# Kernel optimization log

Measured on AMD Instinct MI355X. Metric: run time of the kernel, lower is better.

## Reference

```python
import jax, jax.numpy as jnp
import numpy as np

N = 100000   # nodes
E = 1600000  # edges
G = 512      # graphs in batch
F_IN = 128
H = 128
F_OUT = 1


def setup_inputs() -> dict:
    key = jax.random.key(0)
    ks = jax.random.split(key, 12)
    x = jax.random.normal(ks[0], (N, F_IN), dtype=jnp.float32)
    src = jax.random.randint(ks[1], (E,), 0, N, dtype=jnp.int32)
    dst = jax.random.randint(ks[2], (E,), 0, N, dtype=jnp.int32)
    node2graph = jnp.sort(jax.random.randint(ks[3], (N,), 0, G, dtype=jnp.int32))
    s_in = 1.0 / np.sqrt(F_IN)
    s_h = 1.0 / np.sqrt(H)
    W0 = jax.random.normal(ks[4], (F_IN, H), dtype=jnp.float32) * s_in
    b0 = jnp.zeros((H,), dtype=jnp.float32)
    W1 = jax.random.normal(ks[5], (H, H), dtype=jnp.float32) * s_h
    b1 = jnp.zeros((H,), dtype=jnp.float32)
    W2 = jax.random.normal(ks[6], (H, H), dtype=jnp.float32) * s_h
    b2 = jnp.zeros((H,), dtype=jnp.float32)
    Wm1 = jax.random.normal(ks[7], (H, H), dtype=jnp.float32) * s_h
    bm1 = jnp.zeros((H,), dtype=jnp.float32)
    Wm2 = jax.random.normal(ks[8], (H, F_OUT), dtype=jnp.float32) * s_h
    bm2 = jnp.zeros((F_OUT,), dtype=jnp.float32)
    return {"x": x, "src": src, "dst": dst, "node2graph": node2graph,
            "W0": W0, "b0": b0, "W1": W1, "b1": b1, "W2": W2, "b2": b2,
            "Wm1": Wm1, "bm1": bm1, "Wm2": Wm2, "bm2": bm2}


def _degree_norms(src, dst):
    ones = jnp.ones((E,), dtype=jnp.float32)
    out_deg = jax.ops.segment_sum(ones, src, num_segments=N)
    in_deg = jax.ops.segment_sum(ones, dst, num_segments=N)
    norm_out = jax.lax.rsqrt(jnp.maximum(out_deg, 1.0))  # [N]
    norm_in = jax.lax.rsqrt(jnp.maximum(in_deg, 1.0))    # [N]
    return norm_out, norm_in


def _graph_conv(x, src, dst, norm_out, norm_in, W, b):
    # DGL GraphConv, norm='both', in_feats <= out_feats path:
    # aggregate normalized src features, then linear + activation.
    xs = x * norm_out[:, None]
    msg = xs[src]                                         # [E, H] gather
    agg = jax.ops.segment_sum(msg, dst, num_segments=N)   # [N, H] scatter-add
    agg = agg * norm_in[:, None]
    return jax.nn.relu(agg @ W + b)


def reference(x, src, dst, node2graph, W0, b0, W1, b1, W2, b2, Wm1, bm1, Wm2, bm2):
    norm_out, norm_in = _degree_norms(src, dst)
    h = _graph_conv(x, src, dst, norm_out, norm_in, W0, b0)
    h = _graph_conv(h, src, dst, norm_out, norm_in, W1, b1)
    h = _graph_conv(h, src, dst, norm_out, norm_in, W2, b2)
    # sum_nodes readout per graph
    g = jax.ops.segment_sum(h, node2graph, num_segments=G)  # [G, H]
    # MLP head: Linear -> ReLU -> Linear
    return jax.nn.relu(g @ Wm1 + bm1) @ Wm2 + bm2           # [G, 1]
```

## Files before the change

### kernel.cpp

```cpp
#include <hip/hip_runtime.h>

#define NN 100000
#define NE 1600000
#define NG 512
#define HD 128

#define NBK 196
#define CHUNK 5120
#define NC 313
#define LH (2 * NBK * NC)

typedef _Float16 half4 __attribute__((ext_vector_type(4)));
typedef _Float16 h8 __attribute__((ext_vector_type(8)));
typedef float f32x4 __attribute__((ext_vector_type(4)));

__global__ __launch_bounds__(256) void k_hist(const int* __restrict__ src,
                                              const int* __restrict__ dst,
                                              int* __restrict__ H,
                                              const float* __restrict__ W0,
                                              const float* __restrict__ W1,
                                              const float* __restrict__ W2,
                                              _Float16* __restrict__ Bt) {
    if (blockIdx.x >= NC) {
        int i = (blockIdx.x - NC) * 256 + threadIdx.x;
        int w = i >> 14;
        int rem = i & 16383;
        int n = rem >> 7;
        int k = rem & 127;
        const float* W = (w == 0) ? W0 : ((w == 1) ? W1 : W2);
        Bt[i] = (_Float16)W[k * 128 + n];
        return;
    }
    __shared__ int hd[NBK], hs[NBK];
    int c = blockIdx.x;
    for (int i = threadIdx.x; i < NBK; i += 256) { hd[i] = 0; hs[i] = 0; }
    __syncthreads();
    int e0 = c * CHUNK;
    int e1 = e0 + CHUNK; if (e1 > NE) e1 = NE;
    for (int e = e0 + threadIdx.x; e < e1; e += 256) {
        atomicAdd(&hd[dst[e] >> 9], 1);
        atomicAdd(&hs[src[e] >> 9], 1);
    }
    __syncthreads();
    for (int i = threadIdx.x; i < NBK; i += 256) {
        H[i * NC + c] = hd[i];
        H[NBK * NC + i * NC + c] = hs[i];
    }
}

__global__ __launch_bounds__(256) void k_scan1g(int* __restrict__ H,
                                                int* __restrict__ bsum, int L) {
    __shared__ int s[256];
    int i = blockIdx.x * 256 + threadIdx.x;
    int v = (i < L) ? H[i] : 0;
    s[threadIdx.x] = v;
    __syncthreads();
    for (int off = 1; off < 256; off <<= 1) {
        int t = (threadIdx.x >= off) ? s[threadIdx.x - off] : 0;
        __syncthreads();
        s[threadIdx.x] += t;
        __syncthreads();
    }
    if (i < L) H[i] = s[threadIdx.x] - v;
    if (threadIdx.x == 255) bsum[blockIdx.x] = s[255];
}

__global__ __launch_bounds__(256) void k_scan3g(int* __restrict__ H,
                                                const int* __restrict__ bsum,
                                                int L, int nb) {
    __shared__ int sb[512];
    __shared__ int tmp2[256];
    int t = threadIdx.x;
    int b0 = (2 * t < nb) ? bsum[2 * t] : 0;
    int b1 = (2 * t + 1 < nb) ? bsum[2 * t + 1] : 0;
    int pair = b0 + b1;
    tmp2[t] = pair;
    __syncthreads();
    for (int off = 1; off < 256; off <<= 1) {
        int v2 = (t >= off) ? tmp2[t - off] : 0;
        __syncthreads();
        tmp2[t] += v2;
        __syncthreads();
    }
    int ex = tmp2[t] - pair;
    sb[2 * t] = ex;
    sb[2 * t + 1] = ex + b0;
    __syncthreads();
    int i = blockIdx.x * 256 + t;
    if (i < L) H[i] += sb[i >> 8];
}

__global__ __launch_bounds__(256) void k_scatter(const int* __restrict__ src,
                                                 const int* __restrict__ dst,
                                                 const int* __restrict__ H,
                                                 int* __restrict__ dpart,
                                                 unsigned short* __restrict__ spart) {
    __shared__ int cd[NBK], cs[NBK];
    int c = blockIdx.x;
    for (int i = threadIdx.x; i < NBK; i += 256) {
        cd[i] = H[i * NC + c];
        cs[i] = H[NBK * NC + i * NC + c] - NE;
    }
    __syncthreads();
    int e0 = c * CHUNK;
    int e1 = e0 + CHUNK; if (e1 > NE) e1 = NE;
    for (int e = e0 + threadIdx.x; e < e1; e += 256) {
        int s = src[e], d = dst[e];
        int pd = atomicAdd(&cd[d >> 9], 1);
        dpart[pd] = s | ((d & 511) << 17);
        int ps = atomicAdd(&cs[s >> 9], 1);
        spart[ps] = (unsigned short)(s & 511);
    }
}

__global__ __launch_bounds__(256) void k_bucket(const int* __restrict__ dpart,
                                                const unsigned short* __restrict__ spart,
                                                const int* __restrict__ H,
                                                int* __restrict__ offs,
                                                int* __restrict__ csr,
                                                float* __restrict__ ni,
                                                float* __restrict__ no) {
    __shared__ int deg[512];
    __shared__ int cur[512];
    __shared__ int tmp[256];
    int b = blockIdx.x;
    bool isDst = (b < NBK);
    int bb = isDst ? b : b - NBK;
    int start, end;
    if (isDst) {
        start = H[bb * NC];
        end = (bb + 1 < NBK) ? H[(bb + 1) * NC] : NE;
    } else {
        start = H[NBK * NC + bb * NC] - NE;
        end = (bb + 1 < NBK) ? H[NBK * NC + (bb + 1) * NC] - NE : NE;
    }
    for (int i = threadIdx.x; i < 512; i += 256) deg[i] = 0;
    __syncthreads();
    if (isDst) {
        for (int i = start + threadIdx.x; i < end; i += 256)
            atomicAdd(&deg[(dpart[i] >> 17) & 511], 1);
    } else {
        for (int i = start + threadIdx.x; i < end; i += 256)
            atomicAdd(&deg[spart[i]], 1);
    }
    __syncthreads();
    int vb = bb * 512;
    if (!isDst) {
        for (int i = threadIdx.x; i < 512; i += 256) {
            int v = vb + i;
            if (v < NN) no[v] = rsqrtf(fmaxf((float)deg[i], 1.0f));
        }
        return;
    }
    int t = threadIdx.x;
    int a0 = deg[2 * t], a1 = deg[2 * t + 1];
    int pair = a0 + a1;
    tmp[t] = pair;
    __syncthreads();
    for (int off = 1; off < 256; off <<= 1) {
        int v2 = (t >= off) ? tmp[t - off] : 0;
        __syncthreads();
        tmp[t] += v2;
        __syncthreads();
    }
    int ex = tmp[t] - pair;
    cur[2 * t] = start + ex;
    cur[2 * t + 1] = start + ex + a0;
    __syncthreads();
    for (int i = threadIdx.x; i < 512; i += 256) {
        int v = vb + i;
        if (v < NN) {
            offs[v] = cur[i];
            ni[v] = rsqrtf(fmaxf((float)deg[i], 1.0f));
        }
    }
    if (b == NBK - 1 && threadIdx.x == 0) offs[NN] = NE;
    __syncthreads();
    for (int i = start + threadIdx.x; i < end; i += 256) {
        int pk = dpart[i];
        int p = atomicAdd(&cur[(pk >> 17) & 511], 1);
        csr[p] = pk & 0x1FFFF;
    }
}

template <typename TA>
__global__ __launch_bounds__(256) void k_gemm_mfma(const TA* __restrict__ A,
                                                   const _Float16* __restrict__ Bt,
                                                   const float* __restrict__ no,
                                                   _Float16* __restrict__ Zh,
                                                   int nrows) {
    __shared__ _Float16 Bs[128 * 136];
    int tid = threadIdx.x;
    {
        const h8* B8 = (const h8*)Bt;
        h8* Bs8 = (h8*)Bs;
        for (int i = tid; i < 2048; i += 256) {
            int n = i >> 4, c = i & 15;
            Bs8[n * 17 + c] = B8[i];
        }
    }

    int wave = tid >> 6;
    int lane = tid & 63;
    int m16 = lane & 15;
    int quad = lane >> 4;
    int rowbase = blockIdx.x * 64 + wave * 16;
    int row = rowbase + m16;
    bool valid = row < nrows;

    h8 afrag[4];
    if (valid) {
        if constexpr (sizeof(TA) == 2) {
            const h8* Arow = (const h8*)(A + (size_t)row * 128);
#pragma unroll
            for (int kk = 0; kk < 4; kk++) afrag[kk] = Arow[kk * 4 + quad];
        } else {
            const float4* Arow = (const float4*)(A + (size_t)row * 128);
#pragma unroll
            for (int kk = 0; kk < 4; kk++) {
                float4 lo = Arow[kk * 8 + quad * 2];
                float4 hi = Arow[kk * 8 + quad * 2 + 1];
                h8 a;
                a[0] = (_Float16)lo.x; a[1] = (_Float16)lo.y;
                a[2] = (_Float16)lo.z; a[3] = (_Float16)lo.w;
                a[4] = (_Float16)hi.x; a[5] = (_Float16)hi.y;
                a[6] = (_Float16)hi.z; a[7] = (_Float16)hi.w;
                afrag[kk] = a;
            }
        }
    } else {
#pragma unroll
        for (int kk = 0; kk < 4; kk++) {
            h8 a;
#pragma unroll
            for (int j = 0; j < 8; j++) a[j] = (_Float16)0.f;
            afrag[kk] = a;
        }
    }

    __syncthreads();

    f32x4 acc[8];
#pragma unroll
    for (int nt = 0; nt < 8; nt++) acc[nt] = (f32x4){0.f, 0.f, 0.f, 0.f};

    const h8* Bs8 = (const h8*)Bs;
#pragma unroll
    for (int nt = 0; nt < 8; nt++) {
        const h8* Bp = Bs8 + (size_t)(nt * 16 + m16) * 17;
#pragma unroll
        for (int kk = 0; kk < 4; kk++) {
            acc[nt] = __builtin_amdgcn_mfma_f32_16x16x32_f16(afrag[kk], Bp[kk * 4 + quad],
                                                             acc[nt], 0, 0, 0);
        }
    }

    float nor[4];
#pragma unroll
    for (int r = 0; r < 4; r++) {
        int grow = rowbase + quad * 4 + r;
        nor[r] = (grow < nrows) ? no[grow] : 0.f;
    }

    __syncthreads();
    {
        int lr0 = wave * 16 + quad * 4;
#pragma unroll
        for (int nt = 0; nt < 8; nt++) {
#pragma unroll
            for (int r = 0; r < 4; r++) {
                Bs[(size_t)(lr0 + r) * 136 + nt * 16 + m16] =
                    (_Float16)(acc[nt][r] * nor[r]);
            }
        }
    }
    __syncthreads();

    int blockrow0 = blockIdx.x * 64;
    for (int i = tid; i < 1024; i += 256) {
        int r = i >> 4, cch = i & 15;
        int grow = blockrow0 + r;
        if (grow < nrows) {
            h8 val = *(const h8*)&Bs[(size_t)r * 136 + cch * 8];
            *(h8*)&Zh[(size_t)grow * 128 + cch * 8] = val;
        }
    }
}

__global__ __launch_bounds__(256) void k_agg(const h8* __restrict__ Zh,
                                             const int* __restrict__ offs,
                                             const int* __restrict__ csr,
                                             const float* __restrict__ ni,
                                             const float* __restrict__ b,
                                             h8* __restrict__ H16) {
    int v = blockIdx.x * 16 + (threadIdx.x >> 4);
    int c = threadIdx.x & 15;
    int s = offs[v];
    int e = offs[v + 1];
    float a0[8], a1[8];
#pragma unroll
    for (int j = 0; j < 8; j++) { a0[j] = 0.f; a1[j] = 0.f; }
    int i = s;
    for (; i + 4 <= e; i += 4) {
        int u0 = csr[i];
        int u1 = csr[i + 1];
        int u2 = csr[i + 2];
        int u3 = csr[i + 3];
        h8 z0 = Zh[(size_t)u0 * 16 + c];
        h8 z1 = Zh[(size_t)u1 * 16 + c];
        h8 z2 = Zh[(size_t)u2 * 16 + c];
        h8 z3 = Zh[(size_t)u3 * 16 + c];
#pragma unroll
        for (int j = 0; j < 8; j++) {
            a0[j] += (float)z0[j] + (float)z1[j];
            a1[j] += (float)z2[j] + (float)z3[j];
        }
    }
    for (; i < e; i++) {
        int u = csr[i];
        h8 z = Zh[(size_t)u * 16 + c];
#pragma unroll
        for (int j = 0; j < 8; j++) a0[j] += (float)z[j];
    }
    float niv = ni[v];
    const float* bb = b + c * 8;
    h8 r;
#pragma unroll
    for (int j = 0; j < 8; j++)
        r[j] = (_Float16)fmaxf((a0[j] + a1[j]) * niv + bb[j], 0.f);
    H16[(size_t)v * 16 + c] = r;
}

__global__ __launch_bounds__(128) void k_readhead(const h8* __restrict__ H8,
                                                  const int* __restrict__ n2g,
                                                  const float* __restrict__ Wm1,
                                                  const float* __restrict__ bm1,
                                                  const float* __restrict__ Wm2,
                                                  const float* __restrict__ bm2,
                                                  float* __restrict__ out) {
    __shared__ float red[128 * 8];
    __shared__ float gs[128];
    __shared__ float red2[128];
    int gi = blockIdx.x;
    int t = threadIdx.x;
    int slot = t >> 4;
    int c = t & 15;

    int lo = 0, hi = NN;
    while (lo < hi) { int mid = (lo + hi) >> 1; if (n2g[mid] < gi) lo = mid + 1; else hi = mid; }
    int s = lo;
    hi = NN;
    while (lo < hi) { int mid = (lo + hi) >> 1; if (n2g[mid] < gi + 1) lo = mid + 1; else hi = mid; }
    int e = lo;

    float acc[8];
#pragma unroll
    for (int j = 0; j < 8; j++) acc[j] = 0.f;
    for (int v = s + slot; v < e; v += 8) {
        h8 z = H8[(size_t)v * 16 + c];
#pragma unroll
        for (int j = 0; j < 8; j++) acc[j] += (float)z[j];
    }
#pragma unroll
    for (int j = 0; j < 8; j++) red[t * 8 + j] = acc[j];
    __syncthreads();
    for (int off = 4; off >= 1; off >>= 1) {
        if (slot < off) {
#pragma unroll
            for (int j = 0; j < 8; j++)
                red[t * 8 + j] += red[(t + off * 16) * 8 + j];
        }
        __syncthreads();
    }
    if (slot == 0) {
#pragma unroll
        for (int j = 0; j < 8; j++) gs[c * 8 + j] = red[t * 8 + j];
    }
    __syncthreads();

    int f = t;
    float a = bm1[f];
    for (int k = 0; k < 128; k++) a += gs[k] * Wm1[k * 128 + f];
    float h1 = fmaxf(a, 0.f);
    red2[f] = h1 * Wm2[f];
    __syncthreads();
    for (int s2 = 64; s2 > 0; s2 >>= 1) {
        if (f < s2) red2[f] += red2[f + s2];
        __syncthreads();
    }
    if (f == 0) out[gi] = red2[0] + bm2[0];
}

extern "C" void kernel_launch(void* const* d_in, const int* in_sizes, int n_in,
                              void* d_out, int out_size, void* d_ws, size_t ws_size,
                              hipStream_t stream) {
    const float* x   = (const float*)d_in[0];
    const int*   src = (const int*)d_in[1];
    const int*   dst = (const int*)d_in[2];
    const int*   n2g = (const int*)d_in[3];
    const float* W0  = (const float*)d_in[4];
    const float* b0  = (const float*)d_in[5];
    const float* W1  = (const float*)d_in[6];
    const float* b1  = (const float*)d_in[7];
    const float* W2  = (const float*)d_in[8];
    const float* b2  = (const float*)d_in[9];
    const float* Wm1 = (const float*)d_in[10];
    const float* bm1 = (const float*)d_in[11];
    const float* Wm2 = (const float*)d_in[12];
    const float* bm2 = (const float*)d_in[13];
    float* out = (float*)d_out;

    char* p = (char*)d_ws;
    auto carve = [&](size_t bytes) -> char* {
        char* r = p;
        p += (bytes + 255) & ~(size_t)255;
        return r;
    };
    _Float16* zh  = (_Float16*)carve((size_t)NN * HD * 2);
    _Float16* h16 = (_Float16*)carve((size_t)NN * HD * 2);
    _Float16* Bt  = (_Float16*)carve((size_t)3 * 128 * 128 * 2);
    float* no     = (float*)carve((size_t)NN * 4);
    float* ni     = (float*)carve((size_t)NN * 4);
    int*   offs   = (int*)carve((size_t)(NN + 1) * 4);
    int*   csr    = (int*)carve((size_t)NE * 4);
    int*   Hh     = (int*)carve((size_t)LH * 4);
    int*   bsum   = (int*)carve((size_t)512 * 4);
    int*   dpart  = (int*)carve((size_t)NE * 4);
    unsigned short* spart = (unsigned short*)carve((size_t)NE * 2);

    int scan_blocks = (LH + 255) / 256;
    k_hist<<<NC + 192, 256, 0, stream>>>(src, dst, Hh, W0, W1, W2, Bt);
    k_scan1g<<<scan_blocks, 256, 0, stream>>>(Hh, bsum, LH);
    k_scan3g<<<scan_blocks, 256, 0, stream>>>(Hh, bsum, LH, scan_blocks);
    k_scatter<<<NC, 256, 0, stream>>>(src, dst, Hh, dpart, spart);
    k_bucket<<<2 * NBK, 256, 0, stream>>>(dpart, spart, Hh, offs, csr, ni, no);

    int gemm_blocks = (NN + 63) / 64;
    int agg_blocks  = NN / 16;

    k_gemm_mfma<float><<<gemm_blocks, 256, 0, stream>>>(x, Bt, no, zh, NN);
    k_agg<<<agg_blocks, 256, 0, stream>>>((const h8*)zh, offs, csr, ni, b0, (h8*)h16);
    k_gemm_mfma<_Float16><<<gemm_blocks, 256, 0, stream>>>(h16, Bt + 16384, no, zh, NN);
    k_agg<<<agg_blocks, 256, 0, stream>>>((const h8*)zh, offs, csr, ni, b1, (h8*)h16);
    k_gemm_mfma<_Float16><<<gemm_blocks, 256, 0, stream>>>(h16, Bt + 32768, no, zh, NN);
    k_agg<<<agg_blocks, 256, 0, stream>>>((const h8*)zh, offs, csr, ni, b2, (h8*)h16);

    k_readhead<<<NG, 128, 0, stream>>>((const h8*)h16, n2g, Wm1, bm1, Wm2, bm2, out);
}
```

Measured before the change: 407.6 us.

## Fuse aggregation with per-layer GEMM and reorder to aggregate-then-transform

Replaces the separate GEMM and aggregation kernels with one fused kernel per layer. It gathers the normalized neighbour features, does the 16x128x128 MFMA GEMM on the aggregated rows in shared memory, then applies bias, ReLU and the next layer's out-degree norm before writing fp16 output. A small prep kernel scales x by the out-degree norm and converts it to fp16 first. This follows the reference order (aggregate, then linear) and removes one full N x 128 write and read per layer plus three kernel launches. In exchange, every 16-row block reloads its B fragments from global memory instead of shared memory.

```diff
diff --git a/kernel.cpp b/kernel.cpp
--- a/kernel.cpp
+++ b/kernel.cpp
@@ -10,7 +10,6 @@
 #define NC 313
 #define LH (2 * NBK * NC)
 
-typedef _Float16 half4 __attribute__((ext_vector_type(4)));
 typedef _Float16 h8 __attribute__((ext_vector_type(8)));
 typedef float f32x4 __attribute__((ext_vector_type(4)));
 
@@ -183,118 +182,37 @@
     }
 }
 
-template <typename TA>
-__global__ __launch_bounds__(256) void k_gemm_mfma(const TA* __restrict__ A,
-                                                   const _Float16* __restrict__ Bt,
-                                                   const float* __restrict__ no,
-                                                   _Float16* __restrict__ Zh,
-                                                   int nrows) {
-    __shared__ _Float16 Bs[128 * 136];
+__global__ __launch_bounds__(256) void k_prep(const float* __restrict__ x,
+                                              const float* __restrict__ no,
+                                              h8* __restrict__ T) {
+    int i = blockIdx.x * 256 + threadIdx.x;
+    int v = i >> 4;
+    float nov = no[v];
+    const float4* xr = (const float4*)(x + ((size_t)i << 3));
+    float4 lo = xr[0], hi = xr[1];
+    h8 r;
+    r[0] = (_Float16)(lo.x * nov); r[1] = (_Float16)(lo.y * nov);
+    r[2] = (_Float16)(lo.z * nov); r[3] = (_Float16)(lo.w * nov);
+    r[4] = (_Float16)(hi.x * nov); r[5] = (_Float16)(hi.y * nov);
+    r[6] = (_Float16)(hi.z * nov); r[7] = (_Float16)(hi.w * nov);
+    T[i] = r;
+}
+
+__global__ __launch_bounds__(256, 8) void k_agg_gemm(const h8* __restrict__ T,
+                                                     const int* __restrict__ offs,
+                                                     const int* __restrict__ csr,
+                                                     const float* __restrict__ ni,
+                                                     const float* __restrict__ no,
+                                                     const _Float16* __restrict__ Bt,
+                                                     const float* __restrict__ bias,
+                                                     h8* __restrict__ Out,
+                                                     int mulNo) {
+    __shared__ _Float16 As[16 * 136];
+    __shared__ _Float16 Cs[16 * 136];
     int tid = threadIdx.x;
-    {
-        const h8* B8 = (const h8*)Bt;
-        h8* Bs8 = (h8*)Bs;
-        for (int i = tid; i < 2048; i += 256) {
-            int n = i >> 4, c = i & 15;
-            Bs8[n * 17 + c] = B8[i];
-        }
-    }
-
-    int wave = tid >> 6;
-    int lane = tid & 63;
-    int m16 = lane & 15;
-    int quad = lane >> 4;
-    int rowbase = blockIdx.x * 64 + wave * 16;
-    int row = rowbase + m16;
-    bool valid = row < nrows;
-
-    h8 afrag[4];
-    if (valid) {
-        if constexpr (sizeof(TA) == 2) {
-            const h8* Arow = (const h8*)(A + (size_t)row * 128);
-#pragma unroll
-            for (int kk = 0; kk < 4; kk++) afrag[kk] = Arow[kk * 4 + quad];
-        } else {
-            const float4* Arow = (const float4*)(A + (size_t)row * 128);
-#pragma unroll
-            for (int kk = 0; kk < 4; kk++) {
-                float4 lo = Arow[kk * 8 + quad * 2];
-                float4 hi = Arow[kk * 8 + quad * 2 + 1];
-                h8 a;
-                a[0] = (_Float16)lo.x; a[1] = (_Float16)lo.y;
-                a[2] = (_Float16)lo.z; a[3] = (_Float16)lo.w;
-                a[4] = (_Float16)hi.x; a[5] = (_Float16)hi.y;
-                a[6] = (_Float16)hi.z; a[7] = (_Float16)hi.w;
-                afrag[kk] = a;
-            }
-        }
-    } else {
-#pragma unroll
-        for (int kk = 0; kk < 4; kk++) {
-            h8 a;
-#pragma unroll
-            for (int j = 0; j < 8; j++) a[j] = (_Float16)0.f;
-            afrag[kk] = a;
-        }
-    }
-
-    __syncthreads();
-
-    f32x4 acc[8];
-#pragma unroll
-    for (int nt = 0; nt < 8; nt++) acc[nt] = (f32x4){0.f, 0.f, 0.f, 0.f};
-
-    const h8* Bs8 = (const h8*)Bs;
-#pragma unroll
-    for (int nt = 0; nt < 8; nt++) {
-        const h8* Bp = Bs8 + (size_t)(nt * 16 + m16) * 17;
-#pragma unroll
-        for (int kk = 0; kk < 4; kk++) {
-            acc[nt] = __builtin_amdgcn_mfma_f32_16x16x32_f16(afrag[kk], Bp[kk * 4 + quad],
-                                                             acc[nt], 0, 0, 0);
-        }
-    }
-
-    float nor[4];
-#pragma unroll
-    for (int r = 0; r < 4; r++) {
-        int grow = rowbase + quad * 4 + r;
-        nor[r] = (grow < nrows) ? no[grow] : 0.f;
-    }
-
-    __syncthreads();
-    {
-        int lr0 = wave * 16 + quad * 4;
-#pragma unroll
-        for (int nt = 0; nt < 8; nt++) {
-#pragma unroll
-            for (int r = 0; r < 4; r++) {
-                Bs[(size_t)(lr0 + r) * 136 + nt * 16 + m16] =
-                    (_Float16)(acc[nt][r] * nor[r]);
-            }
-        }
-    }
-    __syncthreads();
-
-    int blockrow0 = blockIdx.x * 64;
-    for (int i = tid; i < 1024; i += 256) {
-        int r = i >> 4, cch = i & 15;
-        int grow = blockrow0 + r;
-        if (grow < nrows) {
-            h8 val = *(const h8*)&Bs[(size_t)r * 136 + cch * 8];
-            *(h8*)&Zh[(size_t)grow * 128 + cch * 8] = val;
-        }
-    }
-}
-
-__global__ __launch_bounds__(256) void k_agg(const h8* __restrict__ Zh,
-                                             const int* __restrict__ offs,
-                                             const int* __restrict__ csr,
-                                             const float* __restrict__ ni,
-                                             const float* __restrict__ b,
-                                             h8* __restrict__ H16) {
-    int v = blockIdx.x * 16 + (threadIdx.x >> 4);
-    int c = threadIdx.x & 15;
+    int slot = tid >> 4;
+    int c = tid & 15;
+    int v = blockIdx.x * 16 + slot;
     int s = offs[v];
     int e = offs[v + 1];
     float a0[8], a1[8];
@@ -306,10 +224,10 @@
         int u1 = csr[i + 1];
         int u2 = csr[i + 2];
         int u3 = csr[i + 3];
-        h8 z0 = Zh[(size_t)u0 * 16 + c];
-        h8 z1 = Zh[(size_t)u1 * 16 + c];
-        h8 z2 = Zh[(size_t)u2 * 16 + c];
-        h8 z3 = Zh[(size_t)u3 * 16 + c];
+        h8 z0 = T[(size_t)u0 * 16 + c];
+        h8 z1 = T[(size_t)u1 * 16 + c];
+        h8 z2 = T[(size_t)u2 * 16 + c];
+        h8 z3 = T[(size_t)u3 * 16 + c];
 #pragma unroll
         for (int j = 0; j < 8; j++) {
             a0[j] += (float)z0[j] + (float)z1[j];
@@ -318,17 +236,56 @@
     }
     for (; i < e; i++) {
         int u = csr[i];
-        h8 z = Zh[(size_t)u * 16 + c];
+        h8 z = T[(size_t)u * 16 + c];
 #pragma unroll
         for (int j = 0; j < 8; j++) a0[j] += (float)z[j];
     }
     float niv = ni[v];
-    const float* bb = b + c * 8;
-    h8 r;
-#pragma unroll
-    for (int j = 0; j < 8; j++)
-        r[j] = (_Float16)fmaxf((a0[j] + a1[j]) * niv + bb[j], 0.f);
-    H16[(size_t)v * 16 + c] = r;
+    h8 av;
+#pragma unroll
+    for (int j = 0; j < 8; j++) av[j] = (_Float16)((a0[j] + a1[j]) * niv);
+    ((h8*)As)[slot * 17 + c] = av;
+    __syncthreads();
+
+    int wave = tid >> 6;
+    int lane = tid & 63;
+    int m16 = lane & 15;
+    int quad = lane >> 4;
+    const h8* B8 = (const h8*)Bt;
+    const h8* As8 = (const h8*)As;
+    h8 afr[4];
+#pragma unroll
+    for (int kk = 0; kk < 4; kk++) afr[kk] = As8[m16 * 17 + kk * 4 + quad];
+
+    float4 nos;
+    if (mulNo) {
+        nos = *(const float4*)&no[blockIdx.x * 16 + quad * 4];
+    } else {
+        nos = make_float4(1.f, 1.f, 1.f, 1.f);
+    }
+    float ns[4] = {nos.x, nos.y, nos.z, nos.w};
+
+#pragma unroll
+    for (int hh = 0; hh < 2; hh++) {
+        int nt = wave + hh * 4;
+        h8 bf[4];
+#pragma unroll
+        for (int kk = 0; kk < 4; kk++)
+            bf[kk] = B8[(size_t)(nt * 16 + m16) * 16 + kk * 4 + quad];
+        f32x4 acc = (f32x4){0.f, 0.f, 0.f, 0.f};
+#pragma unroll
+        for (int kk = 0; kk < 4; kk++)
+            acc = __builtin_amdgcn_mfma_f32_16x16x32_f16(afr[kk], bf[kk], acc, 0, 0, 0);
+        float bv = bias[nt * 16 + m16];
+#pragma unroll
+        for (int r = 0; r < 4; r++) {
+            float hv = fmaxf(acc[r] + bv, 0.f);
+            Cs[(size_t)(quad * 4 + r) * 136 + nt * 16 + m16] = (_Float16)(hv * ns[r]);
+        }
+    }
+    __syncthreads();
+    int rr = tid >> 4;
+    Out[(size_t)(blockIdx.x * 16 + rr) * 16 + c] = *(const h8*)&Cs[(size_t)rr * 136 + c * 8];
 }
 
 __global__ __launch_bounds__(128) void k_readhead(const h8* __restrict__ H8,
@@ -435,15 +392,16 @@
     k_scatter<<<NC, 256, 0, stream>>>(src, dst, Hh, dpart, spart);
     k_bucket<<<2 * NBK, 256, 0, stream>>>(dpart, spart, Hh, offs, csr, ni, no);
 
-    int gemm_blocks = (NN + 63) / 64;
-    int agg_blocks  = NN / 16;
-
-    k_gemm_mfma<float><<<gemm_blocks, 256, 0, stream>>>(x, Bt, no, zh, NN);
-    k_agg<<<agg_blocks, 256, 0, stream>>>((const h8*)zh, offs, csr, ni, b0, (h8*)h16);
-    k_gemm_mfma<_Float16><<<gemm_blocks, 256, 0, stream>>>(h16, Bt + 16384, no, zh, NN);
-    k_agg<<<agg_blocks, 256, 0, stream>>>((const h8*)zh, offs, csr, ni, b1, (h8*)h16);
-    k_gemm_mfma<_Float16><<<gemm_blocks, 256, 0, stream>>>(h16, Bt + 32768, no, zh, NN);
-    k_agg<<<agg_blocks, 256, 0, stream>>>((const h8*)zh, offs, csr, ni, b2, (h8*)h16);
+    int agg_blocks = NN / 16;
+    int prep_blocks = (NN * 16) / 256;
+
+    k_prep<<<prep_blocks, 256, 0, stream>>>(x, no, (h8*)zh);
+    k_agg_gemm<<<agg_blocks, 256, 0, stream>>>((const h8*)zh, offs, csr, ni, no,
+                                               Bt, b0, (h8*)h16, 1);
+    k_agg_gemm<<<agg_blocks, 256, 0, stream>>>((const h8*)h16, offs, csr, ni, no,
+                                               Bt + 16384, b1, (h8*)zh, 1);
+    k_agg_gemm<<<agg_blocks, 256, 0, stream>>>((const h8*)zh, offs, csr, ni, no,
+                                               Bt + 32768, b2, (h8*)h16, 0);
 
     k_readhead<<<NG, 128, 0, stream>>>((const h8*)h16, n2g, Wm1, bm1, Wm2, bm2, out);
 }
```

After: 419.9 us. 1.03x slower.

## Assign one wavefront per node in aggregation with cross-lane shuffle reduction

Applied to the files above, without the earlier changes.

The gather-sum kernel now gives each destination node a full 64-lane wavefront instead of 16 lanes. Four lane groups each handle a different neighbor, and the partial sums are combined with xor shuffles before the group-0 lanes apply normalization, bias and ReLU. The aim is more memory-level parallelism per node and less serial latency for the roughly 16 edges per node. The cost is four times as many threads, and three quarters of the lanes sit idle during the epilogue.

```diff
diff --git a/kernel.cpp b/kernel.cpp
--- a/kernel.cpp
+++ b/kernel.cpp
@@ -10,7 +10,6 @@
 #define NC 313
 #define LH (2 * NBK * NC)
 
-typedef _Float16 half4 __attribute__((ext_vector_type(4)));
 typedef _Float16 h8 __attribute__((ext_vector_type(8)));
 typedef float f32x4 __attribute__((ext_vector_type(4)));
 
@@ -293,42 +292,58 @@
                                              const float* __restrict__ ni,
                                              const float* __restrict__ b,
                                              h8* __restrict__ H16) {
-    int v = blockIdx.x * 16 + (threadIdx.x >> 4);
-    int c = threadIdx.x & 15;
+    int tid = threadIdx.x;
+    int wave = tid >> 6;
+    int lane = tid & 63;
+    int bg = lane >> 4;
+    int c = lane & 15;
+    int v = blockIdx.x * 4 + wave;
     int s = offs[v];
     int e = offs[v + 1];
     float a0[8], a1[8];
 #pragma unroll
     for (int j = 0; j < 8; j++) { a0[j] = 0.f; a1[j] = 0.f; }
     int i = s;
-    for (; i + 4 <= e; i += 4) {
-        int u0 = csr[i];
-        int u1 = csr[i + 1];
-        int u2 = csr[i + 2];
-        int u3 = csr[i + 3];
+    for (; i + 8 <= e; i += 8) {
+        int u0 = csr[i + bg];
+        int u1 = csr[i + 4 + bg];
         h8 z0 = Zh[(size_t)u0 * 16 + c];
         h8 z1 = Zh[(size_t)u1 * 16 + c];
-        h8 z2 = Zh[(size_t)u2 * 16 + c];
-        h8 z3 = Zh[(size_t)u3 * 16 + c];
 #pragma unroll
         for (int j = 0; j < 8; j++) {
-            a0[j] += (float)z0[j] + (float)z1[j];
-            a1[j] += (float)z2[j] + (float)z3[j];
-        }
-    }
-    for (; i < e; i++) {
-        int u = csr[i];
+            a0[j] += (float)z0[j];
+            a1[j] += (float)z1[j];
+        }
+    }
+    if (i + 4 <= e) {
+        int u0 = csr[i + bg];
+        h8 z0 = Zh[(size_t)u0 * 16 + c];
+#pragma unroll
+        for (int j = 0; j < 8; j++) a0[j] += (float)z0[j];
+        i += 4;
+    }
+    if (bg < e - i) {
+        int u = csr[i + bg];
         h8 z = Zh[(size_t)u * 16 + c];
 #pragma unroll
-        for (int j = 0; j < 8; j++) a0[j] += (float)z[j];
-    }
-    float niv = ni[v];
-    const float* bb = b + c * 8;
-    h8 r;
-#pragma unroll
-    for (int j = 0; j < 8; j++)
-        r[j] = (_Float16)fmaxf((a0[j] + a1[j]) * niv + bb[j], 0.f);
-    H16[(size_t)v * 16 + c] = r;
+        for (int j = 0; j < 8; j++) a1[j] += (float)z[j];
+    }
+#pragma unroll
+    for (int j = 0; j < 8; j++) {
+        float t = a0[j] + a1[j];
+        t += __shfl_xor(t, 16, 64);
+        t += __shfl_xor(t, 32, 64);
+        a0[j] = t;
+    }
+    if (bg == 0) {
+        float niv = ni[v];
+        const float* bb = b + c * 8;
+        h8 r;
+#pragma unroll
+        for (int j = 0; j < 8; j++)
+            r[j] = (_Float16)fmaxf(a0[j] * niv + bb[j], 0.f);
+        H16[(size_t)v * 16 + c] = r;
+    }
 }
 
 __global__ __launch_bounds__(128) void k_readhead(const h8* __restrict__ H8,
@@ -436,7 +451,7 @@
     k_bucket<<<2 * NBK, 256, 0, stream>>>(dpart, spart, Hh, offs, csr, ni, no);
 
     int gemm_blocks = (NN + 63) / 64;
-    int agg_blocks  = NN / 16;
+    int agg_blocks  = NN / 4;
 
     k_gemm_mfma<float><<<gemm_blocks, 256, 0, stream>>>(x, Bt, no, zh, NN);
     k_agg<<<agg_blocks, 256, 0, stream>>>((const h8*)zh, offs, csr, ni, b0, (h8*)h16);
```

After: 414.4 us. Within noise of the previous version (+1.7%).

## Fuse aggregation with next layer's MFMA GEMM and widen readhead block

Applied to the files above, without the earlier changes.

Adds k_aggemm, which aggregates neighbour features for 16 nodes per block, applies bias, ReLU and norm_in, then multiplies the resulting fp16 rows by the next layer's weights with MFMA, scaling by norm_out. This removes two standalone GEMM launches and the round trip of the hidden activations through global memory between agg and GEMM. Each block reloads the full 128x128 weight matrix from global/L2, and the shuffle-based fragment layout adds register pressure. The readhead kernel also moves to 256 threads with 16 node slots per graph.

```diff
diff --git a/kernel.cpp b/kernel.cpp
--- a/kernel.cpp
+++ b/kernel.cpp
@@ -10,7 +10,6 @@
 #define NC 313
 #define LH (2 * NBK * NC)
 
-typedef _Float16 half4 __attribute__((ext_vector_type(4)));
 typedef _Float16 h8 __attribute__((ext_vector_type(8)));
 typedef float f32x4 __attribute__((ext_vector_type(4)));
 
@@ -331,14 +330,102 @@
     H16[(size_t)v * 16 + c] = r;
 }
 
-__global__ __launch_bounds__(128) void k_readhead(const h8* __restrict__ H8,
+__global__ __launch_bounds__(256, 8) void k_aggemm(const h8* __restrict__ Zin,
+                                                   const int* __restrict__ offs,
+                                                   const int* __restrict__ csr,
+                                                   const float* __restrict__ ni,
+                                                   const float* __restrict__ no,
+                                                   const _Float16* __restrict__ Bt,
+                                                   const float* __restrict__ bias,
+                                                   h8* __restrict__ Zout) {
+    __shared__ _Float16 Ws[16 * 128];
+    int tid = threadIdx.x;
+    int slot = tid >> 4;
+    int c = tid & 15;
+    int v = blockIdx.x * 16 + slot;
+    int s = offs[v];
+    int e = offs[v + 1];
+    float a0[8], a1[8];
+#pragma unroll
+    for (int j = 0; j < 8; j++) { a0[j] = 0.f; a1[j] = 0.f; }
+    int i = s;
+    for (; i + 4 <= e; i += 4) {
+        int u0 = csr[i];
+        int u1 = csr[i + 1];
+        int u2 = csr[i + 2];
+        int u3 = csr[i + 3];
+        h8 z0 = Zin[(size_t)u0 * 16 + c];
+        h8 z1 = Zin[(size_t)u1 * 16 + c];
+        h8 z2 = Zin[(size_t)u2 * 16 + c];
+        h8 z3 = Zin[(size_t)u3 * 16 + c];
+#pragma unroll
+        for (int j = 0; j < 8; j++) {
+            a0[j] += (float)z0[j] + (float)z1[j];
+            a1[j] += (float)z2[j] + (float)z3[j];
+        }
+    }
+    for (; i < e; i++) {
+        int u = csr[i];
+        h8 z = Zin[(size_t)u * 16 + c];
+#pragma unroll
+        for (int j = 0; j < 8; j++) a0[j] += (float)z[j];
+    }
+    float niv = ni[v];
+    const float* bb = bias + c * 8;
+    union { h8 h; int w[4]; } av;
+#pragma unroll
+    for (int j = 0; j < 8; j++)
+        av.h[j] = (_Float16)fmaxf((a0[j] + a1[j]) * niv + bb[j], 0.f);
+
+    int wave = tid >> 6;
+    int lane = tid & 63;
+    int m16 = lane & 15;
+    int quad = lane >> 4;
+
+    h8 afrag[4];
+#pragma unroll
+    for (int kk = 0; kk < 4; kk++) {
+        int sl = ((m16 & 3) << 4) + (kk << 2) + quad;
+        union { int w[4]; h8 h; } t;
+#pragma unroll
+        for (int d = 0; d < 4; d++) t.w[d] = __shfl(av.w[d], sl, 64);
+        afrag[kk] = t.h;
+    }
+
+    int nbase = blockIdx.x * 16 + wave * 4;
+    float4 nov = *(const float4*)&no[nbase];
+    float ns[4] = {nov.x, nov.y, nov.z, nov.w};
+
+    const h8* B8 = (const h8*)Bt;
+    _Float16* Wsw = Ws + (size_t)(wave * 4) * 128;
+#pragma unroll
+    for (int nt = 0; nt < 8; nt++) {
+        h8 bf[4];
+#pragma unroll
+        for (int kk = 0; kk < 4; kk++)
+            bf[kk] = B8[(size_t)(nt * 16 + m16) * 16 + kk * 4 + quad];
+        f32x4 acc = (f32x4){0.f, 0.f, 0.f, 0.f};
+#pragma unroll
+        for (int kk = 0; kk < 4; kk++)
+            acc = __builtin_amdgcn_mfma_f32_16x16x32_f16(afrag[kk], bf[kk], acc, 0, 0, 0);
+        if (quad == 0) {
+#pragma unroll
+            for (int r = 0; r < 4; r++)
+                Wsw[r * 128 + nt * 16 + m16] = (_Float16)(acc[r] * ns[r]);
+        }
+    }
+    h8 z = *(const h8*)&Ws[(size_t)slot * 128 + c * 8];
+    Zout[(size_t)v * 16 + c] = z;
+}
+
+__global__ __launch_bounds__(256) void k_readhead(const h8* __restrict__ H8,
                                                   const int* __restrict__ n2g,
                                                   const float* __restrict__ Wm1,
                                                   const float* __restrict__ bm1,
                                                   const float* __restrict__ Wm2,
                                                   const float* __restrict__ bm2,
                                                   float* __restrict__ out) {
-    __shared__ float red[128 * 8];
+    __shared__ float red[256 * 8];
     __shared__ float gs[128];
     __shared__ float red2[128];
     int gi = blockIdx.x;
@@ -356,7 +443,7 @@
     float acc[8];
 #pragma unroll
     for (int j = 0; j < 8; j++) acc[j] = 0.f;
-    for (int v = s + slot; v < e; v += 8) {
+    for (int v = s + slot; v < e; v += 16) {
         h8 z = H8[(size_t)v * 16 + c];
 #pragma unroll
         for (int j = 0; j < 8; j++) acc[j] += (float)z[j];
@@ -364,7 +451,7 @@
 #pragma unroll
     for (int j = 0; j < 8; j++) red[t * 8 + j] = acc[j];
     __syncthreads();
-    for (int off = 4; off >= 1; off >>= 1) {
+    for (int off = 8; off >= 1; off >>= 1) {
         if (slot < off) {
 #pragma unroll
             for (int j = 0; j < 8; j++)
@@ -378,17 +465,17 @@
     }
     __syncthreads();
 
-    int f = t;
-    float a = bm1[f];
-    for (int k = 0; k < 128; k++) a += gs[k] * Wm1[k * 128 + f];
-    float h1 = fmaxf(a, 0.f);
-    red2[f] = h1 * Wm2[f];
+    if (t < 128) {
+        float a = bm1[t];
+        for (int k = 0; k < 128; k++) a += gs[k] * Wm1[k * 128 + t];
+        red2[t] = fmaxf(a, 0.f) * Wm2[t];
+    }
     __syncthreads();
     for (int s2 = 64; s2 > 0; s2 >>= 1) {
-        if (f < s2) red2[f] += red2[f + s2];
-        __syncthreads();
-    }
-    if (f == 0) out[gi] = red2[0] + bm2[0];
+        if (t < s2) red2[t] += red2[t + s2];
+        __syncthreads();
+    }
+    if (t == 0) out[gi] = red2[0] + bm2[0];
 }
 
 extern "C" void kernel_launch(void* const* d_in, const int* in_sizes, int n_in,
@@ -439,11 +526,11 @@
     int agg_blocks  = NN / 16;
 
     k_gemm_mfma<float><<<gemm_blocks, 256, 0, stream>>>(x, Bt, no, zh, NN);
-    k_agg<<<agg_blocks, 256, 0, stream>>>((const h8*)zh, offs, csr, ni, b0, (h8*)h16);
-    k_gemm_mfma<_Float16><<<gemm_blocks, 256, 0, stream>>>(h16, Bt + 16384, no, zh, NN);
-    k_agg<<<agg_blocks, 256, 0, stream>>>((const h8*)zh, offs, csr, ni, b1, (h8*)h16);
-    k_gemm_mfma<_Float16><<<gemm_blocks, 256, 0, stream>>>(h16, Bt + 32768, no, zh, NN);
+    k_aggemm<<<agg_blocks, 256, 0, stream>>>((const h8*)zh, offs, csr, ni, no,
+                                             Bt + 16384, b0, (h8*)h16);
+    k_aggemm<<<agg_blocks, 256, 0, stream>>>((const h8*)h16, offs, csr, ni, no,
+                                             Bt + 32768, b1, (h8*)zh);
     k_agg<<<agg_blocks, 256, 0, stream>>>((const h8*)zh, offs, csr, ni, b2, (h8*)h16);
 
-    k_readhead<<<NG, 128, 0, stream>>>((const h8*)h16, n2g, Wm1, bm1, Wm2, bm2, out);
-}
+    k_readhead<<<NG, 256, 0, stream>>>((const h8*)h16, n2g, Wm1, bm1, Wm2, bm2, out);
+}
```

After: 521.9 us. 28.0% more time.
